# Kernel optimization log

Hardware: AMD Instinct MI355X
Metric: run time of the kernel (lower is better)

The kernel has to match this reference:

```python
import jax, jax.numpy as jnp
import numpy as np

N = 4096      # nodes
HID = 512     # hidden_size
HEADS = 8
DH = HID // HEADS
EPS = 1e-5    # BatchNorm eps


def setup_inputs() -> dict:
    key = jax.random.key(0)
    ks = jax.random.split(key, 16)
    h = jax.random.normal(ks[0], (N, HID), jnp.float32)
    # sparse adjacency (~degree 32) with self-loops so every row has a neighbor
    A = (jax.random.uniform(ks[1], (N, N)) < 0.008).astype(jnp.float32)
    A = jnp.maximum(A, jnp.eye(N, dtype=jnp.float32))
    w = lambda k, shp: jax.random.normal(k, shp, jnp.float32) * 0.02
    return {
        "A": A, "h": h,
        "Wq": w(ks[2], (HID, HID)), "bq": jnp.zeros((HID,), jnp.float32),
        "Wk": w(ks[3], (HID, HID)), "bk": jnp.zeros((HID,), jnp.float32),
        "Wv": w(ks[4], (HID, HID)), "bv": jnp.zeros((HID,), jnp.float32),
        "Wo": w(ks[5], (HID, HID)), "bo": jnp.zeros((HID,), jnp.float32),
        "bn1_g": jnp.ones((HID,), jnp.float32), "bn1_b": jnp.zeros((HID,), jnp.float32),
        "bn2_g": jnp.ones((HID,), jnp.float32), "bn2_b": jnp.zeros((HID,), jnp.float32),
        "W1": w(ks[6], (HID, 2 * HID)), "b1": jnp.zeros((2 * HID,), jnp.float32),
        "W2": w(ks[7], (2 * HID, HID)), "b2": jnp.zeros((HID,), jnp.float32),
    }


def _batchnorm(x, g, b):
    # BatchNorm1d training mode: stats over the node (batch) axis
    m = jnp.mean(x, axis=0)
    v = jnp.var(x, axis=0)
    return g * (x - m) * jax.lax.rsqrt(v + EPS) + b


def _layer(A, h, Wq, bq, Wk, bk, Wv, bv, Wo, bo,
           bn1_g, bn1_b, bn2_g, bn2_b, W1, b1, W2, b2):
    n = h.shape[0]
    q = (h @ Wq + bq).reshape(n, HEADS, DH)
    k = (h @ Wk + bk).reshape(n, HEADS, DH)
    v = (h @ Wv + bv).reshape(n, HEADS, DH)
    # scores [heads, n, m], masked by adjacency
    scores = jnp.einsum('nhd,mhd->hnm', q, k) / np.float32(np.sqrt(DH))
    scores = jnp.where(A[None, :, :] > 0, scores, jnp.float32(-1e9))
    attn = jax.nn.softmax(scores, axis=-1)
    o = jnp.einsum('hnm,mhd->nhd', attn, v).reshape(n, HID)
    h1 = o @ Wo + bo
    h = _batchnorm(h + h1, bn1_g, bn1_b)
    h2 = jax.nn.relu(h @ W1 + b1) @ W2 + b2
    return _batchnorm(h + h2, bn2_g, bn2_b)


def reference(A, h, Wq, bq, Wk, bk, Wv, bv, Wo, bo,
              bn1_g, bn1_b, bn2_g, bn2_b, W1, b1, W2, b2):
    return _layer(A, h, Wq, bq, Wk, bk, Wv, bv, Wo, bo,
                  bn1_g, bn1_b, bn2_g, bn2_b, W1, b1, W2, b2)
```

## Files before the change

kernel.cpp:

```cpp
#include <hip/hip_runtime.h>

#define N_NODES 4096
#define HID 512
#define HEADS 8
#define DH 64
#define EPS 1e-5f
#define MAXD 128

typedef __attribute__((ext_vector_type(8))) short bf16x8;
typedef __attribute__((ext_vector_type(4))) float f32x4;

__device__ __forceinline__ unsigned short f2bf(float f) {
    unsigned int u = __float_as_uint(f);
    unsigned int r = (u + 0x7FFFu + ((u >> 16) & 1u)) >> 16;
    return (unsigned short)r;
}
__device__ __forceinline__ float blo(unsigned int u) {
    return __uint_as_float(u << 16);
}
__device__ __forceinline__ float bhi(unsigned int u) {
    return __uint_as_float(u & 0xffff0000u);
}

__device__ __forceinline__ void gld_lds16(const void* g, void* l) {
    __builtin_amdgcn_global_load_lds(
        (const __attribute__((address_space(1))) unsigned int*)g,
        (__attribute__((address_space(3))) unsigned int*)l, 16, 0, 0);
}

template<int BN, int EPI>
__global__ __launch_bounds__(256) void gemm_bf16(
    const unsigned short* __restrict__ Xb, const unsigned short* __restrict__ Wt,
    const float* __restrict__ bias, const float* __restrict__ res,
    float* __restrict__ outf, unsigned short* __restrict__ outb,
    float* __restrict__ sum, float* __restrict__ sumsq,
    int K, int Nc)
{
    constexpr int WM = (BN == 128) ? 4 : 2;
    __shared__ __align__(16) unsigned short As[128 * 32];
    __shared__ __align__(16) unsigned short Bs[BN * 32];

    const int tid = threadIdx.x;
    const int lane = tid & 63;
    const int wv = tid >> 6;
    const int wm = (BN == 128) ? (wv >> 1) : wv;
    const int wn = (BN == 128) ? (wv & 1) : 0;
    const int m0 = blockIdx.y * 128, n0 = blockIdx.x * BN;
    const int lc = lane & 15, lq = lane >> 4;

    const int rowA = tid >> 2;
    const int kof = ((tid & 3) ^ ((tid >> 3) & 3)) * 8;
    unsigned short* ldsA = As + tid * 8;
    unsigned short* ldsB = Bs + tid * 8;

    const int rslot = (lq ^ ((lc >> 1) & 3)) * 8;

    f32x4 acc[WM][4] = {};

    for (int k0 = 0; k0 < K; k0 += 32) {
        const unsigned short* gA = Xb + (size_t)(m0 + rowA) * K + k0 + kof;
        const unsigned short* gB = Wt + (size_t)(n0 + rowA) * K + k0 + kof;
        gld_lds16(gA, ldsA);
        gld_lds16(gA + (size_t)64 * K, ldsA + 2048);
        gld_lds16(gB, ldsB);
        if (BN == 128) gld_lds16(gB + (size_t)64 * K, ldsB + 2048);
        __syncthreads();

        bf16x8 af[WM], bfr[4];
        #pragma unroll
        for (int i = 0; i < WM; ++i)
            af[i] = *(const bf16x8*)&As[(wm * (WM * 16) + i * 16 + lc) * 32 + rslot];
        #pragma unroll
        for (int j = 0; j < 4; ++j)
            bfr[j] = *(const bf16x8*)&Bs[(wn * 64 + j * 16 + lc) * 32 + rslot];
        #pragma unroll
        for (int i = 0; i < WM; ++i)
            #pragma unroll
            for (int j = 0; j < 4; ++j)
                acc[i][j] = __builtin_amdgcn_mfma_f32_16x16x32_bf16(af[i], bfr[j], acc[i][j], 0, 0, 0);
        __syncthreads();
    }

    float cs[4] = {}, css[4] = {};
    #pragma unroll
    for (int i = 0; i < WM; ++i) {
        #pragma unroll
        for (int j = 0; j < 4; ++j) {
            const int gr0 = m0 + wm * (WM * 16) + i * 16 + lq * 4;
            const int gc = n0 + wn * 64 + j * 16 + lc;
            const float bi = bias[gc];
            #pragma unroll
            for (int r = 0; r < 4; ++r) {
                float val = acc[i][j][r] + bi;
                size_t off = (size_t)(gr0 + r) * Nc + gc;
                if (EPI == 0)      outb[off] = f2bf(val);
                else if (EPI == 1) outb[off] = f2bf(fmaxf(val, 0.f));
                else {
                    val += res[off];
                    outf[off] = val;
                    cs[j] += val; css[j] += val * val;
                }
            }
        }
    }
    if (EPI == 2) {
        #pragma unroll
        for (int j = 0; j < 4; ++j) {
            float s = cs[j], ss = css[j];
            s += __shfl_xor(s, 16); s += __shfl_xor(s, 32);
            ss += __shfl_xor(ss, 16); ss += __shfl_xor(ss, 32);
            if (lq == 0) {
                const int gc = n0 + wn * 64 + j * 16 + lc;
                atomicAdd(&sum[gc], s);
                atomicAdd(&sumsq[gc], ss);
            }
        }
    }
}

__global__ __launch_bounds__(256) void conv_bf16v(
    const float4* __restrict__ in, unsigned int* __restrict__ out, int n4)
{
    int i = blockIdx.x * 256 + threadIdx.x;
    if (i < n4) {
        float4 f = in[i];
        out[i * 2]     = (unsigned int)f2bf(f.x) | ((unsigned int)f2bf(f.y) << 16);
        out[i * 2 + 1] = (unsigned int)f2bf(f.z) | ((unsigned int)f2bf(f.w) << 16);
    }
}

__global__ __launch_bounds__(256) void transpose_all(
    const float* __restrict__ Wq, const float* __restrict__ Wk,
    const float* __restrict__ Wv, const float* __restrict__ Wo,
    const float* __restrict__ W1, const float* __restrict__ W2,
    unsigned short* __restrict__ wqkvT, unsigned short* __restrict__ woT,
    unsigned short* __restrict__ w1T, unsigned short* __restrict__ w2T)
{
    const float* in; unsigned short* out; int R, C;
    switch (blockIdx.z) {
        case 0: in = Wq; out = wqkvT;          R = 512;  C = 512;  break;
        case 1: in = Wk; out = wqkvT + 262144; R = 512;  C = 512;  break;
        case 2: in = Wv; out = wqkvT + 524288; R = 512;  C = 512;  break;
        case 3: in = Wo; out = woT;            R = 512;  C = 512;  break;
        case 4: in = W1; out = w1T;            R = 512;  C = 1024; break;
        default: in = W2; out = w2T;           R = 1024; C = 512;  break;
    }
    const int bc = blockIdx.x * 32, br = blockIdx.y * 32;
    if (bc >= C || br >= R) return;
    __shared__ float tile[32][33];
    const int tx = threadIdx.x & 31, ty = threadIdx.x >> 5;
    #pragma unroll
    for (int r = ty; r < 32; r += 8)
        tile[r][tx] = in[(size_t)(br + r) * C + bc + tx];
    __syncthreads();
    #pragma unroll
    for (int r = ty; r < 32; r += 8)
        out[(size_t)(bc + r) * R + br + tx] = f2bf(tile[tx][r]);
}

__global__ __launch_bounds__(256) void concat_bias(
    const float* __restrict__ bq, const float* __restrict__ bk,
    const float* __restrict__ bv, float* __restrict__ out)
{
    int i = blockIdx.x * 256 + threadIdx.x;
    out[i] = i < 512 ? bq[i] : (i < 1024 ? bk[i - 512] : bv[i - 1024]);
}

__global__ __launch_bounds__(256) void build_adj(
    const float* __restrict__ A, int* __restrict__ idx, int* __restrict__ deg)
{
    int row = (blockIdx.x * 256 + threadIdx.x) >> 6;
    int lane = threadIdx.x & 63;
    if (row >= N_NODES) return;
    const float4* r4 = (const float4*)(A + (size_t)row * N_NODES);
    int base = 0;
    for (int c0 = 0; c0 < N_NODES; c0 += 256) {
        float4 v = r4[(c0 >> 2) + lane];
        #pragma unroll
        for (int b = 0; b < 4; ++b) {
            float vb = (b == 0) ? v.x : (b == 1) ? v.y : (b == 2) ? v.z : v.w;
            unsigned long long m = __ballot(vb > 0.0f);
            int before = __popcll(m & ((1ull << lane) - 1ull));
            if (vb > 0.0f) {
                int p = base + before;
                if (p < MAXD) idx[row * MAXD + p] = c0 + lane * 4 + b;
            }
            base += __popcll(m);
        }
    }
    if (lane == 0) deg[row] = base < MAXD ? base : MAXD;
}

__global__ __launch_bounds__(256) void sparse_attn4(
    const unsigned short* __restrict__ qkv, const int* __restrict__ idx,
    const int* __restrict__ deg, unsigned short* __restrict__ o)
{
    const int n = blockIdx.x;
    const int tid = threadIdx.x;
    const int wv = tid >> 6, lane = tid & 63;

    __shared__ int s_idx[MAXD];
    __shared__ float s_p[8][MAXD];

    const int d = deg[n];
    for (int i = tid; i < d; i += 256) s_idx[i] = idx[n * MAXD + i];
    __syncthreads();

    const int jl = lane >> 3;
    const int dgs = lane & 7;
    const int jl2 = lane >> 4;
    const int dga = lane & 15;

    const int h0 = wv, h1 = wv + 4;

    const unsigned short* qp = qkv + (size_t)n * 1536 + dgs * 8;
    uint4 qa = *(const uint4*)(qp + h0 * 64);
    uint4 qb = *(const uint4*)(qp + h1 * 64);
    const float a0 = blo(qa.x), a1 = bhi(qa.x), a2 = blo(qa.y), a3 = bhi(qa.y);
    const float a4 = blo(qa.z), a5 = bhi(qa.z), a6 = blo(qa.w), a7 = bhi(qa.w);
    const float b0 = blo(qb.x), b1 = bhi(qb.x), b2 = blo(qb.y), b3 = bhi(qb.y);
    const float b4 = blo(qb.z), b5 = bhi(qb.z), b6 = blo(qb.w), b7 = bhi(qb.w);

    uint4 ka = {0, 0, 0, 0}, kb = {0, 0, 0, 0};
    if (jl < d) {
        const unsigned short* p = qkv + (size_t)s_idx[jl] * 1536 + 512 + dgs * 8;
        ka = *(const uint4*)(p + h0 * 64);
        kb = *(const uint4*)(p + h1 * 64);
    }
    for (int j0 = 0; j0 < d; j0 += 8) {
        const uint4 ca = ka, cb = kb;
        const int jn = j0 + 8 + jl;
        if (jn < d) {
            const unsigned short* p = qkv + (size_t)s_idx[jn] * 1536 + 512 + dgs * 8;
            ka = *(const uint4*)(p + h0 * 64);
            kb = *(const uint4*)(p + h1 * 64);
        }
        const int jc = j0 + jl;
        float s0 = 0.f, s1 = 0.f;
        if (jc < d) {
            s0 = a0 * blo(ca.x) + a1 * bhi(ca.x) + a2 * blo(ca.y) + a3 * bhi(ca.y)
               + a4 * blo(ca.z) + a5 * bhi(ca.z) + a6 * blo(ca.w) + a7 * bhi(ca.w);
            s1 = b0 * blo(cb.x) + b1 * bhi(cb.x) + b2 * blo(cb.y) + b3 * bhi(cb.y)
               + b4 * blo(cb.z) + b5 * bhi(cb.z) + b6 * blo(cb.w) + b7 * bhi(cb.w);
        }
        s0 += __shfl_xor(s0, 1); s1 += __shfl_xor(s1, 1);
        s0 += __shfl_xor(s0, 2); s1 += __shfl_xor(s1, 2);
        s0 += __shfl_xor(s0, 4); s1 += __shfl_xor(s1, 4);
        if (dgs == 0 && jc < d) {
            s_p[h0][jc] = s0 * 0.125f;
            s_p[h1][jc] = s1 * 0.125f;
        }
    }

    float inv0, inv1;
    #pragma unroll
    for (int hh = 0; hh < 2; ++hh) {
        float* sp = s_p[hh ? h1 : h0];
        float mx = -1e30f;
        for (int j = lane; j < d; j += 64) mx = fmaxf(mx, sp[j]);
        #pragma unroll
        for (int off = 32; off; off >>= 1) mx = fmaxf(mx, __shfl_xor(mx, off));
        float sum = 0.f;
        for (int j = lane; j < d; j += 64) {
            float e = __expf(sp[j] - mx);
            sp[j] = e;
            sum += e;
        }
        #pragma unroll
        for (int off = 32; off; off >>= 1) sum += __shfl_xor(sum, off);
        if (hh) inv1 = 1.0f / sum; else inv0 = 1.0f / sum;
    }

    float x0 = 0.f, x1 = 0.f, x2 = 0.f, x3 = 0.f;
    float y0 = 0.f, y1 = 0.f, y2 = 0.f, y3 = 0.f;
    uint2 va = {0, 0}, vb = {0, 0};
    if (jl2 < d) {
        const unsigned short* p = qkv + (size_t)s_idx[jl2] * 1536 + 1024 + dga * 4;
        va = *(const uint2*)(p + h0 * 64);
        vb = *(const uint2*)(p + h1 * 64);
    }
    for (int j0 = 0; j0 < d; j0 += 4) {
        const uint2 ca = va, cb = vb;
        const int jn = j0 + 4 + jl2;
        if (jn < d) {
            const unsigned short* p = qkv + (size_t)s_idx[jn] * 1536 + 1024 + dga * 4;
            va = *(const uint2*)(p + h0 * 64);
            vb = *(const uint2*)(p + h1 * 64);
        }
        const int jc = j0 + jl2;
        if (jc < d) {
            const float p0 = s_p[h0][jc], p1 = s_p[h1][jc];
            x0 += p0 * blo(ca.x); x1 += p0 * bhi(ca.x);
            x2 += p0 * blo(ca.y); x3 += p0 * bhi(ca.y);
            y0 += p1 * blo(cb.x); y1 += p1 * bhi(cb.x);
            y2 += p1 * blo(cb.y); y3 += p1 * bhi(cb.y);
        }
    }
    x0 += __shfl_xor(x0, 16); x0 += __shfl_xor(x0, 32);
    x1 += __shfl_xor(x1, 16); x1 += __shfl_xor(x1, 32);
    x2 += __shfl_xor(x2, 16); x2 += __shfl_xor(x2, 32);
    x3 += __shfl_xor(x3, 16); x3 += __shfl_xor(x3, 32);
    y0 += __shfl_xor(y0, 16); y0 += __shfl_xor(y0, 32);
    y1 += __shfl_xor(y1, 16); y1 += __shfl_xor(y1, 32);
    y2 += __shfl_xor(y2, 16); y2 += __shfl_xor(y2, 32);
    y3 += __shfl_xor(y3, 16); y3 += __shfl_xor(y3, 32);
    if (jl2 == 0) {
        uint2 w0, w1;
        w0.x = (unsigned int)f2bf(x0 * inv0) | ((unsigned int)f2bf(x1 * inv0) << 16);
        w0.y = (unsigned int)f2bf(x2 * inv0) | ((unsigned int)f2bf(x3 * inv0) << 16);
        w1.x = (unsigned int)f2bf(y0 * inv1) | ((unsigned int)f2bf(y1 * inv1) << 16);
        w1.y = (unsigned int)f2bf(y2 * inv1) | ((unsigned int)f2bf(y3 * inv1) << 16);
        *(uint2*)(o + (size_t)n * 512 + h0 * 64 + dga * 4) = w0;
        *(uint2*)(o + (size_t)n * 512 + h1 * 64 + dga * 4) = w1;
    }
}

__global__ __launch_bounds__(256) void bn_apply4(
    const float4* __restrict__ x, const float* __restrict__ sum,
    const float* __restrict__ sumsq, const float* __restrict__ g,
    const float* __restrict__ b, float4* __restrict__ yf,
    uint2* __restrict__ yb)
{
    const int i = blockIdx.x * 256 + threadIdx.x;
    const int c4 = i & 127;
    const float4 s4 = ((const float4*)sum)[c4];
    const float4 q4 = ((const float4*)sumsq)[c4];
    const float4 g4 = ((const float4*)g)[c4];
    const float4 b4 = ((const float4*)b)[c4];
    const float4 xv = x[i];
    const float kN = 1.0f / N_NODES;
    float4 r;
    {
        float m = s4.x * kN; r.x = g4.x * (xv.x - m) * rsqrtf(q4.x * kN - m * m + EPS) + b4.x;
    }
    {
        float m = s4.y * kN; r.y = g4.y * (xv.y - m) * rsqrtf(q4.y * kN - m * m + EPS) + b4.y;
    }
    {
        float m = s4.z * kN; r.z = g4.z * (xv.z - m) * rsqrtf(q4.z * kN - m * m + EPS) + b4.z;
    }
    {
        float m = s4.w * kN; r.w = g4.w * (xv.w - m) * rsqrtf(q4.w * kN - m * m + EPS) + b4.w;
    }
    yf[i] = r;
    if (yb) {
        uint2 p;
        p.x = (unsigned int)f2bf(r.x) | ((unsigned int)f2bf(r.y) << 16);
        p.y = (unsigned int)f2bf(r.z) | ((unsigned int)f2bf(r.w) << 16);
        yb[i] = p;
    }
}


extern "C" void kernel_launch(void* const* d_in, const int* in_sizes, int n_in,
                              void* d_out, int out_size, void* d_ws, size_t ws_size,
                              hipStream_t stream)
{
    const float* A   = (const float*)d_in[0];
    const float* h   = (const float*)d_in[1];
    const float* Wq  = (const float*)d_in[2];
    const float* bq  = (const float*)d_in[3];
    const float* Wk  = (const float*)d_in[4];
    const float* bk  = (const float*)d_in[5];
    const float* Wv  = (const float*)d_in[6];
    const float* bv  = (const float*)d_in[7];
    const float* Wo  = (const float*)d_in[8];
    const float* bo  = (const float*)d_in[9];
    const float* g1  = (const float*)d_in[10];
    const float* b1g = (const float*)d_in[11];
    const float* g2  = (const float*)d_in[12];
    const float* b2g = (const float*)d_in[13];
    const float* W1  = (const float*)d_in[14];
    const float* b1  = (const float*)d_in[15];
    const float* W2  = (const float*)d_in[16];
    const float* b2  = (const float*)d_in[17];
    float* out = (float*)d_out;

    float* ws = (float*)d_ws;
    unsigned short* hb    = (unsigned short*)(ws);
    unsigned short* qkvb  = (unsigned short*)(ws + 1048576);
    unsigned short* o_bf  = (unsigned short*)(ws + 4194304);
    unsigned short* wqkvT = (unsigned short*)(ws + 5242880);
    unsigned short* woT   = (unsigned short*)(ws + 5636096);
    unsigned short* w1T   = (unsigned short*)(ws + 5767168);
    unsigned short* w2T   = (unsigned short*)(ws + 6029312);
    unsigned short* t_b   = (unsigned short*)(ws + 6291456);
    float* x1   = ws + 8388608;
    float* x2   = ws + 10485760;
    unsigned short* xb1_b = (unsigned short*)(ws + 12582912);
    float* bqkv = ws + 13631488;
    float* st   = ws + 13633024;
    int*   adj  = (int*)(ws + 13635072);
    int*   deg  = adj + N_NODES * MAXD;

    hipMemsetAsync(st, 0, 2048 * sizeof(float), stream);
    conv_bf16v<<<dim3(2048), dim3(256), 0, stream>>>(
        (const float4*)h, (unsigned int*)hb, N_NODES * HID / 4);
    transpose_all<<<dim3(32, 32, 6), dim3(256), 0, stream>>>(
        Wq, Wk, Wv, Wo, W1, W2, wqkvT, woT, w1T, w2T);
    concat_bias<<<dim3(6), dim3(256), 0, stream>>>(bq, bk, bv, bqkv);
    build_adj<<<dim3(N_NODES / 4), dim3(256), 0, stream>>>(A, adj, deg);

    gemm_bf16<128, 0><<<dim3(12, 32), dim3(256), 0, stream>>>(
        hb, wqkvT, bqkv, nullptr, nullptr, qkvb, nullptr, nullptr, 512, 1536);

    sparse_attn4<<<dim3(N_NODES), dim3(256), 0, stream>>>(qkvb, adj, deg, o_bf);

    gemm_bf16<64, 2><<<dim3(8, 32), dim3(256), 0, stream>>>(
        o_bf, woT, bo, h, x1, nullptr, st, st + 512, 512, 512);

    bn_apply4<<<dim3(2048), dim3(256), 0, stream>>>(
        (const float4*)x1, st, st + 512, g1, b1g, (float4*)x1, (uint2*)xb1_b);

    gemm_bf16<128, 1><<<dim3(8, 32), dim3(256), 0, stream>>>(
        xb1_b, w1T, b1, nullptr, nullptr, t_b, nullptr, nullptr, 512, 1024);
    gemm_bf16<64, 2><<<dim3(8, 32), dim3(256), 0, stream>>>(
        t_b, w2T, b2, x1, x2, nullptr, st + 1024, st + 1536, 1024, 512);

    bn_apply4<<<dim3(2048), dim3(256), 0, stream>>>(
        (const float4*)x2, st + 1024, st + 1536, g2, b2g, (float4*)out, nullptr);

    (void)in_sizes; (void)n_in; (void)out_size; (void)ws_size;
}
```

Baseline: 258.7 us.

## Fuse prep kernels, build adjacency inside attention, use 64-wide K tiles in GEMM

```diff
diff --git a/kernel.cpp b/kernel.cpp
--- a/kernel.cpp
+++ b/kernel.cpp
@@ -37,8 +37,8 @@
     int K, int Nc)
 {
     constexpr int WM = (BN == 128) ? 4 : 2;
-    __shared__ __align__(16) unsigned short As[128 * 32];
-    __shared__ __align__(16) unsigned short Bs[BN * 32];
+    __shared__ __align__(16) unsigned short As[128 * 64];
+    __shared__ __align__(16) unsigned short Bs[BN * 64];
 
     const int tid = threadIdx.x;
     const int lane = tid & 63;
@@ -48,36 +48,43 @@
     const int m0 = blockIdx.y * 128, n0 = blockIdx.x * BN;
     const int lc = lane & 15, lq = lane >> 4;
 
-    const int rowA = tid >> 2;
-    const int kof = ((tid & 3) ^ ((tid >> 3) & 3)) * 8;
+    const int srow = tid >> 3;
+    const int schunk = (tid & 7) ^ (srow & 7);
     unsigned short* ldsA = As + tid * 8;
     unsigned short* ldsB = Bs + tid * 8;
 
-    const int rslot = (lq ^ ((lc >> 1) & 3)) * 8;
+    const int rs0 = lq ^ (lc & 7);
+    const int rs1 = (4 + lq) ^ (lc & 7);
 
     f32x4 acc[WM][4] = {};
 
-    for (int k0 = 0; k0 < K; k0 += 32) {
-        const unsigned short* gA = Xb + (size_t)(m0 + rowA) * K + k0 + kof;
-        const unsigned short* gB = Wt + (size_t)(n0 + rowA) * K + k0 + kof;
-        gld_lds16(gA, ldsA);
-        gld_lds16(gA + (size_t)64 * K, ldsA + 2048);
-        gld_lds16(gB, ldsB);
-        if (BN == 128) gld_lds16(gB + (size_t)64 * K, ldsB + 2048);
+    for (int k0 = 0; k0 < K; k0 += 64) {
+        const unsigned short* gA = Xb + (size_t)(m0 + srow) * K + k0 + schunk * 8;
+        const unsigned short* gB = Wt + (size_t)(n0 + srow) * K + k0 + schunk * 8;
+        #pragma unroll
+        for (int p = 0; p < 4; ++p)
+            gld_lds16(gA + (size_t)(p * 32) * K, ldsA + p * 2048);
+        #pragma unroll
+        for (int p = 0; p < BN / 32; ++p)
+            gld_lds16(gB + (size_t)(p * 32) * K, ldsB + p * 2048);
         __syncthreads();
 
-        bf16x8 af[WM], bfr[4];
-        #pragma unroll
-        for (int i = 0; i < WM; ++i)
-            af[i] = *(const bf16x8*)&As[(wm * (WM * 16) + i * 16 + lc) * 32 + rslot];
-        #pragma unroll
-        for (int j = 0; j < 4; ++j)
-            bfr[j] = *(const bf16x8*)&Bs[(wn * 64 + j * 16 + lc) * 32 + rslot];
-        #pragma unroll
-        for (int i = 0; i < WM; ++i)
+        #pragma unroll
+        for (int h = 0; h < 2; ++h) {
+            const int rs = h ? rs1 : rs0;
+            bf16x8 af[WM], bfr[4];
+            #pragma unroll
+            for (int i = 0; i < WM; ++i)
+                af[i] = *(const bf16x8*)&As[(wm * (WM * 16) + i * 16 + lc) * 64 + rs * 8];
             #pragma unroll
             for (int j = 0; j < 4; ++j)
-                acc[i][j] = __builtin_amdgcn_mfma_f32_16x16x32_bf16(af[i], bfr[j], acc[i][j], 0, 0, 0);
+                bfr[j] = *(const bf16x8*)&Bs[(wn * 64 + j * 16 + lc) * 64 + rs * 8];
+            #pragma unroll
+            for (int i = 0; i < WM; ++i)
+                #pragma unroll
+                for (int j = 0; j < 4; ++j)
+                    acc[i][j] = __builtin_amdgcn_mfma_f32_16x16x32_bf16(af[i], bfr[j], acc[i][j], 0, 0, 0);
+        }
         __syncthreads();
     }
 
@@ -118,82 +125,61 @@
     }
 }
 
-__global__ __launch_bounds__(256) void conv_bf16v(
-    const float4* __restrict__ in, unsigned int* __restrict__ out, int n4)
-{
-    int i = blockIdx.x * 256 + threadIdx.x;
-    if (i < n4) {
-        float4 f = in[i];
-        out[i * 2]     = (unsigned int)f2bf(f.x) | ((unsigned int)f2bf(f.y) << 16);
-        out[i * 2 + 1] = (unsigned int)f2bf(f.z) | ((unsigned int)f2bf(f.w) << 16);
-    }
-}
-
-__global__ __launch_bounds__(256) void transpose_all(
+__global__ __launch_bounds__(256) void prep_all(
     const float* __restrict__ Wq, const float* __restrict__ Wk,
     const float* __restrict__ Wv, const float* __restrict__ Wo,
     const float* __restrict__ W1, const float* __restrict__ W2,
+    const float* __restrict__ h,
+    const float* __restrict__ bq, const float* __restrict__ bk,
+    const float* __restrict__ bv,
     unsigned short* __restrict__ wqkvT, unsigned short* __restrict__ woT,
-    unsigned short* __restrict__ w1T, unsigned short* __restrict__ w2T)
+    unsigned short* __restrict__ w1T, unsigned short* __restrict__ w2T,
+    unsigned int* __restrict__ hb, float* __restrict__ bqkv,
+    float* __restrict__ st)
 {
-    const float* in; unsigned short* out; int R, C;
-    switch (blockIdx.z) {
-        case 0: in = Wq; out = wqkvT;          R = 512;  C = 512;  break;
-        case 1: in = Wk; out = wqkvT + 262144; R = 512;  C = 512;  break;
-        case 2: in = Wv; out = wqkvT + 524288; R = 512;  C = 512;  break;
-        case 3: in = Wo; out = woT;            R = 512;  C = 512;  break;
-        case 4: in = W1; out = w1T;            R = 512;  C = 1024; break;
-        default: in = W2; out = w2T;           R = 1024; C = 512;  break;
-    }
-    const int bc = blockIdx.x * 32, br = blockIdx.y * 32;
-    if (bc >= C || br >= R) return;
-    __shared__ float tile[32][33];
-    const int tx = threadIdx.x & 31, ty = threadIdx.x >> 5;
-    #pragma unroll
-    for (int r = ty; r < 32; r += 8)
-        tile[r][tx] = in[(size_t)(br + r) * C + bc + tx];
-    __syncthreads();
-    #pragma unroll
-    for (int r = ty; r < 32; r += 8)
-        out[(size_t)(bc + r) * R + br + tx] = f2bf(tile[tx][r]);
-}
-
-__global__ __launch_bounds__(256) void concat_bias(
-    const float* __restrict__ bq, const float* __restrict__ bk,
-    const float* __restrict__ bv, float* __restrict__ out)
-{
-    int i = blockIdx.x * 256 + threadIdx.x;
-    out[i] = i < 512 ? bq[i] : (i < 1024 ? bk[i - 512] : bv[i - 1024]);
-}
-
-__global__ __launch_bounds__(256) void build_adj(
-    const float* __restrict__ A, int* __restrict__ idx, int* __restrict__ deg)
-{
-    int row = (blockIdx.x * 256 + threadIdx.x) >> 6;
-    int lane = threadIdx.x & 63;
-    if (row >= N_NODES) return;
-    const float4* r4 = (const float4*)(A + (size_t)row * N_NODES);
-    int base = 0;
-    for (int c0 = 0; c0 < N_NODES; c0 += 256) {
-        float4 v = r4[(c0 >> 2) + lane];
-        #pragma unroll
-        for (int b = 0; b < 4; ++b) {
-            float vb = (b == 0) ? v.x : (b == 1) ? v.y : (b == 2) ? v.z : v.w;
-            unsigned long long m = __ballot(vb > 0.0f);
-            int before = __popcll(m & ((1ull << lane) - 1ull));
-            if (vb > 0.0f) {
-                int p = base + before;
-                if (p < MAXD) idx[row * MAXD + p] = c0 + lane * 4 + b;
-            }
-            base += __popcll(m);
-        }
-    }
-    if (lane == 0) deg[row] = base < MAXD ? base : MAXD;
-}
-
-__global__ __launch_bounds__(256) void sparse_attn4(
-    const unsigned short* __restrict__ qkv, const int* __restrict__ idx,
-    const int* __restrict__ deg, unsigned short* __restrict__ o)
+    const int z = blockIdx.z;
+    if (z < 6) {
+        const float* in; unsigned short* out; int R, C;
+        switch (z) {
+            case 0: in = Wq; out = wqkvT;          R = 512;  C = 512;  break;
+            case 1: in = Wk; out = wqkvT + 262144; R = 512;  C = 512;  break;
+            case 2: in = Wv; out = wqkvT + 524288; R = 512;  C = 512;  break;
+            case 3: in = Wo; out = woT;            R = 512;  C = 512;  break;
+            case 4: in = W1; out = w1T;            R = 512;  C = 1024; break;
+            default: in = W2; out = w2T;           R = 1024; C = 512;  break;
+        }
+        const int bc = blockIdx.x * 32, br = blockIdx.y * 32;
+        if (bc >= C || br >= R) return;
+        __shared__ float tile[32][33];
+        const int tx = threadIdx.x & 31, ty = threadIdx.x >> 5;
+        #pragma unroll
+        for (int r = ty; r < 32; r += 8)
+            tile[r][tx] = in[(size_t)(br + r) * C + bc + tx];
+        __syncthreads();
+        #pragma unroll
+        for (int r = ty; r < 32; r += 8)
+            out[(size_t)(bc + r) * R + br + tx] = f2bf(tile[tx][r]);
+    } else if (z == 6) {
+        const int blk = blockIdx.y * 32 + blockIdx.x;
+        const int i = blk * 512 + threadIdx.x * 2;
+        const float4* in4 = (const float4*)h;
+        #pragma unroll
+        for (int u = 0; u < 2; ++u) {
+            float4 f = in4[i + u];
+            hb[(i + u) * 2]     = (unsigned int)f2bf(f.x) | ((unsigned int)f2bf(f.y) << 16);
+            hb[(i + u) * 2 + 1] = (unsigned int)f2bf(f.z) | ((unsigned int)f2bf(f.w) << 16);
+        }
+    } else {
+        const int blk = blockIdx.y * 32 + blockIdx.x;
+        const int i = blk * 256 + threadIdx.x;
+        if (i < 1536) bqkv[i] = i < 512 ? bq[i] : (i < 1024 ? bk[i - 512] : bv[i - 1024]);
+        if (i < 2048) st[i] = 0.0f;
+    }
+}
+
+__global__ __launch_bounds__(256) void sparse_attn5(
+    const float* __restrict__ A, const unsigned short* __restrict__ qkv,
+    unsigned short* __restrict__ o)
 {
     const int n = blockIdx.x;
     const int tid = threadIdx.x;
@@ -201,16 +187,52 @@
 
     __shared__ int s_idx[MAXD];
     __shared__ float s_p[8][MAXD];
-
-    const int d = deg[n];
-    for (int i = tid; i < d; i += 256) s_idx[i] = idx[n * MAXD + i];
+    __shared__ int s_cnt[4];
+
+    const float4* r4 = (const float4*)(A + (size_t)n * N_NODES);
+    float4 av[4];
+    #pragma unroll
+    for (int t = 0; t < 4; ++t)
+        av[t] = r4[wv * 256 + t * 64 + lane];
+
+    const unsigned long long lt = (1ull << lane) - 1ull;
+    int cnt = 0;
+    #pragma unroll
+    for (int t = 0; t < 4; ++t) {
+        #pragma unroll
+        for (int b = 0; b < 4; ++b) {
+            float vb = (b == 0) ? av[t].x : (b == 1) ? av[t].y : (b == 2) ? av[t].z : av[t].w;
+            cnt += __popcll(__ballot(vb > 0.0f));
+        }
+    }
+    if (lane == 0) s_cnt[wv] = cnt;
+    __syncthreads();
+    int base = 0, total = 0;
+    #pragma unroll
+    for (int w = 0; w < 4; ++w) {
+        if (w < wv) base += s_cnt[w];
+        total += s_cnt[w];
+    }
+    const int d = total < MAXD ? total : MAXD;
+    #pragma unroll
+    for (int t = 0; t < 4; ++t) {
+        #pragma unroll
+        for (int b = 0; b < 4; ++b) {
+            float vb = (b == 0) ? av[t].x : (b == 1) ? av[t].y : (b == 2) ? av[t].z : av[t].w;
+            unsigned long long m = __ballot(vb > 0.0f);
+            if (vb > 0.0f) {
+                int p = base + __popcll(m & lt);
+                if (p < MAXD) s_idx[p] = wv * 1024 + t * 256 + lane * 4 + b;
+            }
+            base += __popcll(m);
+        }
+    }
     __syncthreads();
 
     const int jl = lane >> 3;
     const int dgs = lane & 7;
     const int jl2 = lane >> 4;
     const int dga = lane & 15;
-
     const int h0 = wv, h1 = wv + 4;
 
     const unsigned short* qp = qkv + (size_t)n * 1536 + dgs * 8;
@@ -330,18 +352,10 @@
     const float4 xv = x[i];
     const float kN = 1.0f / N_NODES;
     float4 r;
-    {
-        float m = s4.x * kN; r.x = g4.x * (xv.x - m) * rsqrtf(q4.x * kN - m * m + EPS) + b4.x;
-    }
-    {
-        float m = s4.y * kN; r.y = g4.y * (xv.y - m) * rsqrtf(q4.y * kN - m * m + EPS) + b4.y;
-    }
-    {
-        float m = s4.z * kN; r.z = g4.z * (xv.z - m) * rsqrtf(q4.z * kN - m * m + EPS) + b4.z;
-    }
-    {
-        float m = s4.w * kN; r.w = g4.w * (xv.w - m) * rsqrtf(q4.w * kN - m * m + EPS) + b4.w;
-    }
+    { float m = s4.x * kN; r.x = g4.x * (xv.x - m) * rsqrtf(q4.x * kN - m * m + EPS) + b4.x; }
+    { float m = s4.y * kN; r.y = g4.y * (xv.y - m) * rsqrtf(q4.y * kN - m * m + EPS) + b4.y; }
+    { float m = s4.z * kN; r.z = g4.z * (xv.z - m) * rsqrtf(q4.z * kN - m * m + EPS) + b4.z; }
+    { float m = s4.w * kN; r.w = g4.w * (xv.w - m) * rsqrtf(q4.w * kN - m * m + EPS) + b4.w; }
     yf[i] = r;
     if (yb) {
         uint2 p;
@@ -390,21 +404,15 @@
     unsigned short* xb1_b = (unsigned short*)(ws + 12582912);
     float* bqkv = ws + 13631488;
     float* st   = ws + 13633024;
-    int*   adj  = (int*)(ws + 13635072);
-    int*   deg  = adj + N_NODES * MAXD;
-
-    hipMemsetAsync(st, 0, 2048 * sizeof(float), stream);
-    conv_bf16v<<<dim3(2048), dim3(256), 0, stream>>>(
-        (const float4*)h, (unsigned int*)hb, N_NODES * HID / 4);
-    transpose_all<<<dim3(32, 32, 6), dim3(256), 0, stream>>>(
-        Wq, Wk, Wv, Wo, W1, W2, wqkvT, woT, w1T, w2T);
-    concat_bias<<<dim3(6), dim3(256), 0, stream>>>(bq, bk, bv, bqkv);
-    build_adj<<<dim3(N_NODES / 4), dim3(256), 0, stream>>>(A, adj, deg);
+
+    prep_all<<<dim3(32, 32, 8), dim3(256), 0, stream>>>(
+        Wq, Wk, Wv, Wo, W1, W2, h, bq, bk, bv,
+        wqkvT, woT, w1T, w2T, (unsigned int*)hb, bqkv, st);
 
     gemm_bf16<128, 0><<<dim3(12, 32), dim3(256), 0, stream>>>(
         hb, wqkvT, bqkv, nullptr, nullptr, qkvb, nullptr, nullptr, 512, 1536);
 
-    sparse_attn4<<<dim3(N_NODES), dim3(256), 0, stream>>>(qkvb, adj, deg, o_bf);
+    sparse_attn5<<<dim3(N_NODES), dim3(256), 0, stream>>>(A, qkvb, o_bf);
 
     gemm_bf16<64, 2><<<dim3(8, 32), dim3(256), 0, stream>>>(
         o_bf, woT, bo, h, x1, nullptr, st, st + 512, 512, 512);
```

Result: faster. 242.5 us (-6.3%).
